# Kernel optimization log

Measured on AMD Instinct MI355X. Metric: run time of the kernel, lower is better.

Reference implementation:

```python
import jax, jax.numpy as jnp
import numpy as np

N_USERS = 200000
N_ITEMS = 50000
N_ENTITIES = 150000
N_RELATIONS = 32
N_EDGES = 2000000
N_INTER = 1000000
N_HOPS = 2
D = 64


def setup_inputs() -> dict:
    key = jax.random.key(0)
    ks = jax.random.split(key, 10)
    return {
        "user_emb": jax.random.normal(ks[0], (N_USERS, D), jnp.float32) * 0.1,
        "entity_emb": jax.random.normal(ks[1], (N_ENTITIES, D), jnp.float32) * 0.1,
        "weight": jax.random.normal(ks[2], (N_RELATIONS, D), jnp.float32) * 0.1,
        "g1_w": jax.random.normal(ks[3], (D, D), jnp.float32) * 0.1,
        "g2_w": jax.random.normal(ks[4], (D, D), jnp.float32) * 0.1,
        "edge_head": jax.random.randint(ks[5], (N_EDGES,), 0, N_ENTITIES),
        "edge_tail": jax.random.randint(ks[6], (N_EDGES,), 0, N_ENTITIES),
        "edge_type": jax.random.randint(ks[7], (N_EDGES,), 0, N_RELATIONS),
        "mat_row": jax.random.randint(ks[8], (N_INTER,), 0, N_USERS),
        "mat_col": jax.random.randint(ks[9], (N_INTER,), 0, N_ITEMS),
    }


def _scatter_mean(src, index, num_segments):
    s = jax.ops.segment_sum(src, index, num_segments=num_segments)
    cnt = jax.ops.segment_sum(jnp.ones((src.shape[0],), src.dtype), index,
                              num_segments=num_segments)
    return s / jnp.maximum(cnt, 1.0)[:, None]


def _l2norm(x, eps=1e-12):
    n = jnp.sqrt(jnp.sum(x * x, axis=-1, keepdims=True))
    return x / jnp.maximum(n, eps)


def reference(user_emb, entity_emb, weight, g1_w, g2_w,
              edge_head, edge_tail, edge_type, mat_row, mat_col):
    entity_res = entity_emb
    user_res = user_emb
    item_kg_res = jnp.zeros((N_ITEMS, D), entity_emb.dtype)
    item_int_res = jnp.zeros((N_ITEMS, D), entity_emb.dtype)

    for _ in range(N_HOPS):
        # KG aggregation: gather tail embs, modulate by relation emb, scatter-mean to head
        neigh = entity_emb[edge_tail] * weight[edge_type]            # [E, D]
        entity_agg = _scatter_mean(neigh, edge_head, N_ENTITIES)      # [n_ent, D]
        item_kg_agg = entity_agg[:N_ITEMS]
        att_kg_agg = entity_agg[N_ITEMS:]
        # interaction aggregation: mean of user embs per item
        item_int_agg = _scatter_mean(user_emb[mat_row], mat_col, N_ITEMS)
        # gated fusion (F.linear: x @ W.T)
        gi = jax.nn.sigmoid(item_kg_agg @ g1_w.T + item_int_agg @ g2_w.T)
        item_fusion = gi * item_kg_agg + (1.0 - gi) * item_int_agg
        # user_agg = sparse.mm(user_item, item_fusion) == segment-sum over rows
        user_agg = jax.ops.segment_sum(item_fusion[mat_col], mat_row,
                                       num_segments=N_USERS)
        entity_emb = _l2norm(jnp.concatenate([item_fusion, att_kg_agg], axis=0))
        user_emb = _l2norm(user_agg)
        item_kg_n = _l2norm(item_kg_agg)
        item_int_n = _l2norm(item_int_agg)
        entity_res = entity_res + entity_emb
        user_res = user_res + user_emb
        item_kg_res = item_kg_res + item_kg_n
        item_int_res = item_int_res + item_int_n

    return (entity_res, user_res, item_kg_res, item_int_res)
```

## Files before the change

### kernel.cpp

```cpp
#include <hip/hip_runtime.h>
#include <math.h>

#define N_USERS    200000
#define N_ITEMS    50000
#define N_ENTITIES 150000
#define N_EDGES    2000000
#define N_INTER    1000000
#define D          64

#define CHUNK      1250
#define THR_OWN    5
#define NBLK_E     120
#define NBLK_C     40
#define NBLK_R     160
#define NBLK_TOT   (NBLK_E + NBLK_C + NBLK_R)

#define RK     16384
#define NS     16
#define NR_E   10
#define NR_C   4
#define NR_R   13
#define NR_TOT (NR_E + NR_C + NR_R)
#define KTOT   (N_ENTITIES + N_ITEMS + N_USERS)

#define EB     2048
#define IB     1024

#define FT    64
#define FPAD  132
#define NTILE ((N_ITEMS + FT - 1) / FT)

__device__ __forceinline__ unsigned short f2bf(float f) {
    unsigned u = __float_as_uint(f);
    u += 0x7FFFu + ((u >> 16) & 1u);
    return (unsigned short)(u >> 16);
}
__device__ __forceinline__ ushort4 f2bf4(float4 f) {
    ushort4 o;
    o.x = f2bf(f.x); o.y = f2bf(f.y); o.z = f2bf(f.z); o.w = f2bf(f.w);
    return o;
}
__device__ __forceinline__ float4 bf2f4(ushort4 h) {
    float4 f;
    f.x = __uint_as_float(((unsigned)h.x) << 16);
    f.y = __uint_as_float(((unsigned)h.y) << 16);
    f.z = __uint_as_float(((unsigned)h.z) << 16);
    f.w = __uint_as_float(((unsigned)h.w) << 16);
    return f;
}

__device__ __forceinline__ float qsum16(float v) {
#pragma unroll
    for (int off = 1; off < 16; off <<= 1) v += __shfl_xor(v, off, 64);
    return v;
}

__global__ void cvt2_k(const float4* __restrict__ a, ushort4* __restrict__ ab, int na4,
                       const float4* __restrict__ b, ushort4* __restrict__ bb, int nb4) {
    int n = na4 + nb4;
    for (int i = blockIdx.x * blockDim.x + threadIdx.x; i < n;
         i += gridDim.x * blockDim.x) {
        if (i < na4) ab[i] = f2bf4(a[i]);
        else         bb[i - na4] = f2bf4(b[i - na4]);
    }
}

__global__ void pack_k(const int* __restrict__ tail, const int* __restrict__ type,
                       int* __restrict__ packed) {
    for (int i = blockIdx.x * blockDim.x + threadIdx.x; i < N_EDGES;
         i += gridDim.x * blockDim.x) {
        packed[i] = tail[i] | (type[i] << 18);
    }
}

__device__ __forceinline__ void range_geom(int r, const int*& src, int& n,
                                           int& base, int& cbase, int& rlen,
                                           const int* head, const int* mcol,
                                           const int* mrow) {
    if (r < NR_E) {
        src = head; n = N_EDGES; base = r * RK; cbase = 0;
        rlen = N_ENTITIES - base;
    } else if (r < NR_E + NR_C) {
        src = mcol; n = N_INTER; base = (r - NR_E) * RK;
        cbase = N_ENTITIES; rlen = N_ITEMS - base;
    } else {
        src = mrow; n = N_INTER; base = (r - NR_E - NR_C) * RK;
        cbase = N_ENTITIES + N_ITEMS; rlen = N_USERS - base;
    }
    if (rlen > RK) rlen = RK;
}

__global__ void hist_part_k(const int* __restrict__ head,
                            const int* __restrict__ mcol,
                            const int* __restrict__ mrow,
                            int* __restrict__ partial) {
    __shared__ int lh[RK];
    int r = blockIdx.x >> 4, s = blockIdx.x & (NS - 1);
    for (int d = threadIdx.x; d < RK; d += 256) lh[d] = 0;
    __syncthreads();
    const int* src; int n, base, cbase, rlen;
    range_geom(r, src, n, base, cbase, rlen, head, mcol, mrow);
    int chunk = n / NS;
    int lo = s * chunk, hi = lo + chunk;
    int i = lo + threadIdx.x;
    for (; i + 768 < hi; i += 1024) {
        unsigned d0 = (unsigned)(__builtin_nontemporal_load(&src[i])       - base);
        unsigned d1 = (unsigned)(__builtin_nontemporal_load(&src[i + 256]) - base);
        unsigned d2 = (unsigned)(__builtin_nontemporal_load(&src[i + 512]) - base);
        unsigned d3 = (unsigned)(__builtin_nontemporal_load(&src[i + 768]) - base);
        if (d0 < (unsigned)RK) atomicAdd(&lh[d0], 1);
        if (d1 < (unsigned)RK) atomicAdd(&lh[d1], 1);
        if (d2 < (unsigned)RK) atomicAdd(&lh[d2], 1);
        if (d3 < (unsigned)RK) atomicAdd(&lh[d3], 1);
    }
    for (; i < hi; i += 256) {
        unsigned d = (unsigned)(__builtin_nontemporal_load(&src[i]) - base);
        if (d < (unsigned)RK) atomicAdd(&lh[d], 1);
    }
    __syncthreads();
    int* dst = partial + (size_t)s * KTOT + cbase + base;
    for (int d = threadIdx.x; d < rlen; d += 256) dst[d] = lh[d];
}

__global__ void scanA_k(const int* __restrict__ partial,
                        int* __restrict__ blk_sums) {
    __shared__ int ss[256];
    int b = blockIdx.x, t = threadIdx.x;
    int base = b * CHUNK;
    int sum = 0;
    if (t < 250) {
        int g = base + t * THR_OWN;
#pragma unroll
        for (int s = 0; s < NS; ++s) {
            const int* p = partial + (size_t)s * KTOT + g;
#pragma unroll
            for (int j = 0; j < THR_OWN; ++j) sum += p[j];
        }
    }
    ss[t] = sum;
    __syncthreads();
    for (int off = 128; off > 0; off >>= 1) {
        if (t < off) ss[t] += ss[t + off];
        __syncthreads();
    }
    if (t == 0) blk_sums[b] = ss[0];
}

__global__ void scanB_k(int* __restrict__ blk_sums, int* __restrict__ blk_off,
                        int* __restrict__ e_starts, int* __restrict__ c_starts,
                        int* __restrict__ r_starts) {
    __shared__ int ss[512];
    int t = threadIdx.x;
    ss[t] = (t < NBLK_TOT) ? blk_sums[t] : 0;
    __syncthreads();
    for (int off = 1; off < 512; off <<= 1) {
        int v = (t >= off) ? ss[t - off] : 0;
        __syncthreads();
        ss[t] += v;
        __syncthreads();
    }
    if (t < NBLK_TOT) {
        int excl = (t == 0) ? 0 : ss[t - 1];
        int segstart_excl;
        if (t < NBLK_E) segstart_excl = 0;
        else if (t < NBLK_E + NBLK_C) segstart_excl = ss[NBLK_E - 1];
        else segstart_excl = ss[NBLK_E + NBLK_C - 1];
        blk_off[t] = excl - segstart_excl;
    }
    if (t == 0) {
        e_starts[N_ENTITIES] = N_EDGES;
        c_starts[N_ITEMS]    = N_INTER;
        r_starts[N_USERS]    = N_INTER;
    }
}

__global__ void scanC_k(const int* __restrict__ partial,
                        const int* __restrict__ blk_off,
                        int* __restrict__ e_starts, int* __restrict__ c_starts,
                        int* __restrict__ r_starts,
                        int* __restrict__ e_curs, int* __restrict__ c_curs,
                        int* __restrict__ r_curs) {
    __shared__ int ss[256];
    int b = blockIdx.x, t = threadIdx.x;
    int base = b * CHUNK;
    int tot[THR_OWN];
    int sum = 0;
    if (t < 250) {
        int g = base + t * THR_OWN;
#pragma unroll
        for (int j = 0; j < THR_OWN; ++j) tot[j] = 0;
#pragma unroll
        for (int s = 0; s < NS; ++s) {
            const int* p = partial + (size_t)s * KTOT + g;
#pragma unroll
            for (int j = 0; j < THR_OWN; ++j) tot[j] += p[j];
        }
#pragma unroll
        for (int j = 0; j < THR_OWN; ++j) sum += tot[j];
    }
    ss[t] = sum;
    __syncthreads();
    for (int off = 1; off < 256; off <<= 1) {
        int v = (t >= off) ? ss[t - off] : 0;
        __syncthreads();
        ss[t] += v;
        __syncthreads();
    }
    if (t < 250) {
        int run = blk_off[b] + ((t == 0) ? 0 : ss[t - 1]);
        int* sarr; int* carr; int ebase;
        if (b < NBLK_E)               { sarr = e_starts; carr = e_curs; ebase = base; }
        else if (b < NBLK_E + NBLK_C) { sarr = c_starts; carr = c_curs; ebase = base - NBLK_E * CHUNK; }
        else                          { sarr = r_starts; carr = r_curs; ebase = base - (NBLK_E + NBLK_C) * CHUNK; }
        int gl = ebase + t * THR_OWN;
#pragma unroll
        for (int j = 0; j < THR_OWN; ++j) {
            sarr[gl + j] = run;
            carr[gl + j] = run;
            run += tot[j];
        }
    }
}

__global__ void permute_e_k(const int* __restrict__ head,
                            const int* __restrict__ packed,
                            int* __restrict__ ec, int* __restrict__ e_sorted) {
    int xcd = blockIdx.x & 7;
    int slot = blockIdx.x >> 3;
    int nslot = gridDim.x >> 3;
    int lo = xcd * (N_ENTITIES / 8);
    int hi = lo + (N_ENTITIES / 8);
    for (int i = slot * blockDim.x + threadIdx.x; i < N_EDGES;
         i += nslot * blockDim.x) {
        int h = __builtin_nontemporal_load(&head[i]);
        if (h >= lo && h < hi) {
            int pos = atomicAdd(&ec[h], 1);
            e_sorted[pos] = __builtin_nontemporal_load(&packed[i]);
        }
    }
}

__global__ void permute_i_k(const int* __restrict__ mcol, const int* __restrict__ mrow,
                            int* __restrict__ cc, int* __restrict__ rc,
                            int* __restrict__ i_srow, int* __restrict__ i_scol) {
    int xcd = blockIdx.x & 7;
    int slot = blockIdx.x >> 3;
    int nslot = gridDim.x >> 3;
    int clo = xcd * (N_ITEMS / 8), chi = clo + (N_ITEMS / 8);
    int rlo = xcd * (N_USERS / 8), rhi = rlo + (N_USERS / 8);
    for (int i = slot * blockDim.x + threadIdx.x; i < N_INTER;
         i += nslot * blockDim.x) {
        int c = __builtin_nontemporal_load(&mcol[i]);
        int r = __builtin_nontemporal_load(&mrow[i]);
        if (c >= clo && c < chi) {
            int pos = atomicAdd(&cc[c], 1);
            i_srow[pos] = r;
        }
        if (r >= rlo && r < rhi) {
            int pos = atomicAdd(&rc[r], 1);
            i_scol[pos] = c;
        }
    }
}

__global__ void agg_all_k(const ushort4* __restrict__ ent_bf,
                          const float* __restrict__ ent0f,
                          const float* __restrict__ wrel,
                          const int* __restrict__ es,
                          const int* __restrict__ e_sorted,
                          float* __restrict__ agg,
                          ushort4* __restrict__ ent_cur_bf,
                          float* __restrict__ ent_res,
                          const ushort4* __restrict__ usr_bf,
                          const int* __restrict__ cs,
                          const int* __restrict__ i_srow,
                          float* __restrict__ iint,
                          int first) {
    int lane = threadIdx.x & 63;
    int q = lane >> 4, ql = lane & 15;
    int qb = lane & 48;
    if (blockIdx.x < EB) {
        __shared__ float4 wl4[32 * 16];
        for (int idx = threadIdx.x; idx < 512; idx += 256)
            wl4[idx] = ((const float4*)wrel)[idx];
        __syncthreads();
        int qid = (blockIdx.x * 4 + (threadIdx.x >> 6)) * 4 + q;
        int nq = EB * 16;
        for (int h = qid; h < N_ENTITIES; h += nq) {
            int beg = es[h], end = es[h + 1];
            float4 a0 = {0, 0, 0, 0}, a1 = {0, 0, 0, 0};
            for (int j0 = beg; j0 < end; j0 += 16) {
                int p = (j0 + ql < end) ? e_sorted[j0 + ql] : 0;
                int mm = end - j0; if (mm > 16) mm = 16;
                int k = 0;
                for (; k + 1 < mm; k += 2) {
                    int p0 = __shfl(p, qb | k, 64);
                    int p1 = __shfl(p, qb | (k + 1), 64);
                    float4 e0 = bf2f4(ent_bf[(size_t)(p0 & 0x3FFFF) * 16 + ql]);
                    float4 w0 = wl4[((p0 >> 18) << 4) + ql];
                    float4 e1 = bf2f4(ent_bf[(size_t)(p1 & 0x3FFFF) * 16 + ql]);
                    float4 w1 = wl4[((p1 >> 18) << 4) + ql];
                    a0.x = fmaf(e0.x, w0.x, a0.x); a0.y = fmaf(e0.y, w0.y, a0.y);
                    a0.z = fmaf(e0.z, w0.z, a0.z); a0.w = fmaf(e0.w, w0.w, a0.w);
                    a1.x = fmaf(e1.x, w1.x, a1.x); a1.y = fmaf(e1.y, w1.y, a1.y);
                    a1.z = fmaf(e1.z, w1.z, a1.z); a1.w = fmaf(e1.w, w1.w, a1.w);
                }
                if (k < mm) {
                    int p0 = __shfl(p, qb | k, 64);
                    float4 e0 = bf2f4(ent_bf[(size_t)(p0 & 0x3FFFF) * 16 + ql]);
                    float4 w0 = wl4[((p0 >> 18) << 4) + ql];
                    a0.x = fmaf(e0.x, w0.x, a0.x); a0.y = fmaf(e0.y, w0.y, a0.y);
                    a0.z = fmaf(e0.z, w0.z, a0.z); a0.w = fmaf(e0.w, w0.w, a0.w);
                }
            }
            float4 v; v.x = a0.x + a1.x; v.y = a0.y + a1.y;
            v.z = a0.z + a1.z; v.w = a0.w + a1.w;
            if (h < N_ITEMS) {
                int d = end - beg;
                float inv = 1.0f / (float)(d > 0 ? d : 1);
                float4 o; o.x = v.x * inv; o.y = v.y * inv;
                o.z = v.z * inv; o.w = v.w * inv;
                ((float4*)agg)[(size_t)h * 16 + ql] = o;
            } else {
                float s = qsum16(fmaf(v.x, v.x, fmaf(v.y, v.y, fmaf(v.z, v.z, v.w * v.w))));
                float inv = 1.0f / fmaxf(sqrtf(s), 1e-12f);
                float4 vn; vn.x = v.x * inv; vn.y = v.y * inv;
                vn.z = v.z * inv; vn.w = v.w * inv;
                size_t o4 = (size_t)h * 16 + ql;
                if (first) {
                    ent_cur_bf[o4] = f2bf4(vn);
                    float4 b = ((const float4*)ent0f)[o4];
                    b.x += vn.x; b.y += vn.y; b.z += vn.z; b.w += vn.w;
                    ((float4*)ent_res)[o4] = b;
                } else {
                    float4 r = ((float4*)ent_res)[o4];
                    r.x += vn.x; r.y += vn.y; r.z += vn.z; r.w += vn.w;
                    ((float4*)ent_res)[o4] = r;
                }
            }
        }
    } else {
        int qid = ((blockIdx.x - EB) * 4 + (threadIdx.x >> 6)) * 4 + q;
        int nq = IB * 16;
        for (int c = qid; c < N_ITEMS; c += nq) {
            int beg = cs[c], end = cs[c + 1];
            float4 a0 = {0, 0, 0, 0}, a1 = {0, 0, 0, 0};
            for (int j0 = beg; j0 < end; j0 += 16) {
                int p = (j0 + ql < end) ? i_srow[j0 + ql] : 0;
                int mm = end - j0; if (mm > 16) mm = 16;
                int k = 0;
                for (; k + 1 < mm; k += 2) {
                    int p0 = __shfl(p, qb | k, 64);
                    int p1 = __shfl(p, qb | (k + 1), 64);
                    float4 u0 = bf2f4(usr_bf[(size_t)p0 * 16 + ql]);
                    float4 u1 = bf2f4(usr_bf[(size_t)p1 * 16 + ql]);
                    a0.x += u0.x; a0.y += u0.y; a0.z += u0.z; a0.w += u0.w;
                    a1.x += u1.x; a1.y += u1.y; a1.z += u1.z; a1.w += u1.w;
                }
                if (k < mm) {
                    int p0 = __shfl(p, qb | k, 64);
                    float4 u0 = bf2f4(usr_bf[(size_t)p0 * 16 + ql]);
                    a0.x += u0.x; a0.y += u0.y; a0.z += u0.z; a0.w += u0.w;
                }
            }
            float4 v; v.x = a0.x + a1.x; v.y = a0.y + a1.y;
            v.z = a0.z + a1.z; v.w = a0.w + a1.w;
            int d = end - beg;
            float inv = 1.0f / (float)(d > 0 ? d : 1);
            float4 o; o.x = v.x * inv; o.y = v.y * inv;
            o.z = v.z * inv; o.w = v.w * inv;
            ((float4*)iint)[(size_t)c * 16 + ql] = o;
        }
    }
}

__global__ void fuse_k(const float* __restrict__ agg,
                       const float* __restrict__ iint,
                       const float* __restrict__ g1,
                       const float* __restrict__ g2,
                       const float* __restrict__ ent0,
                       unsigned short* __restrict__ ifus_bf,
                       unsigned short* __restrict__ ent_cur_bf,
                       float* __restrict__ ent_res,
                       float* __restrict__ kg_res,
                       float* __restrict__ int_res,
                       int first) {
    __shared__ float A[FT * FPAD];
    __shared__ float B[64 * FPAD];
    int t = threadIdx.x;
    int ibase = blockIdx.x * FT;

    {
        const float4* g14 = (const float4*)g1;
        const float4* g24 = (const float4*)g2;
        const float4* a4 = (const float4*)(agg + (size_t)ibase * D);
        const float4* i4 = (const float4*)(iint + (size_t)ibase * D);
        for (int idx = t; idx < 1024; idx += 256) {
            int r = idx >> 4, kq = idx & 15;
            ((float4*)&B[r * FPAD])[kq]      = g14[idx];
            ((float4*)&B[r * FPAD + 64])[kq] = g24[idx];
            ((float4*)&A[r * FPAD])[kq]      = a4[idx];
            ((float4*)&A[r * FPAD + 64])[kq] = i4[idx];
        }
    }
    __syncthreads();

    int ti = t >> 4, tj = t & 15;

    float y[4][4] = {};
    for (int k = 0; k < 128; k += 4) {
        float4 av[4], bv[4];
#pragma unroll
        for (int a = 0; a < 4; ++a) av[a] = *(const float4*)&A[(ti + 16 * a) * FPAD + k];
#pragma unroll
        for (int b = 0; b < 4; ++b) bv[b] = *(const float4*)&B[(tj + 16 * b) * FPAD + k];
#pragma unroll
        for (int a = 0; a < 4; ++a)
#pragma unroll
            for (int b = 0; b < 4; ++b) {
                y[a][b] = fmaf(av[a].x, bv[b].x, y[a][b]);
                y[a][b] = fmaf(av[a].y, bv[b].y, y[a][b]);
                y[a][b] = fmaf(av[a].z, bv[b].z, y[a][b]);
                y[a][b] = fmaf(av[a].w, bv[b].w, y[a][b]);
            }
    }

    float fus[4][4], kg[4][4], ii[4][4];
    float sf[4], sk[4], si[4];
#pragma unroll
    for (int a = 0; a < 4; ++a) { sf[a] = 0.f; sk[a] = 0.f; si[a] = 0.f; }
#pragma unroll
    for (int a = 0; a < 4; ++a) {
        int i = ti + 16 * a;
#pragma unroll
        for (int b = 0; b < 4; ++b) {
            int j = tj + 16 * b;
            float K = A[i * FPAD + j];
            float I = A[i * FPAD + 64 + j];
            float gi = 1.0f / (1.0f + __expf(-y[a][b]));
            float f = gi * K + (1.0f - gi) * I;
            fus[a][b] = f; kg[a][b] = K; ii[a][b] = I;
            sf[a] = fmaf(f, f, sf[a]);
            sk[a] = fmaf(K, K, sk[a]);
            si[a] = fmaf(I, I, si[a]);
        }
    }
#pragma unroll
    for (int off = 1; off < 16; off <<= 1) {
#pragma unroll
        for (int a = 0; a < 4; ++a) {
            sf[a] += __shfl_xor(sf[a], off, 64);
            sk[a] += __shfl_xor(sk[a], off, 64);
            si[a] += __shfl_xor(si[a], off, 64);
        }
    }

#pragma unroll
    for (int a = 0; a < 4; ++a) {
        int i = ibase + ti + 16 * a;
        if (i < N_ITEMS) {
            float nf = 1.0f / fmaxf(sqrtf(sf[a]), 1e-12f);
            float nk = 1.0f / fmaxf(sqrtf(sk[a]), 1e-12f);
            float ni = 1.0f / fmaxf(sqrtf(si[a]), 1e-12f);
#pragma unroll
            for (int b = 0; b < 4; ++b) {
                size_t o = (size_t)i * D + tj + 16 * b;
                float f = fus[a][b];
                ifus_bf[o] = f2bf(f);
                float fn = f * nf;
                ent_cur_bf[o] = f2bf(fn);
                if (first) {
                    ent_res[o] = ent0[o] + fn;
                    kg_res[o]  = kg[a][b] * nk;
                    int_res[o] = ii[a][b] * ni;
                } else {
                    ent_res[o] += fn;
                    kg_res[o]  += kg[a][b] * nk;
                    int_res[o] += ii[a][b] * ni;
                }
            }
        }
    }
}

__global__ void user_agg_k(const ushort4* __restrict__ ifus_bf,
                           const int* __restrict__ rs,
                           const int* __restrict__ i_scol,
                           const float* __restrict__ usr0,
                           ushort4* __restrict__ usr_cur_bf,
                           float* __restrict__ usr_res,
                           int first) {
    const float4* u04 = (const float4*)usr0;
    int lane = threadIdx.x & 63;
    int q = lane >> 4, ql = lane & 15;
    int qb = lane & 48;
    int qid = (blockIdx.x * (blockDim.x >> 6) + (threadIdx.x >> 6)) * 4 + q;
    int nq = gridDim.x * (blockDim.x >> 6) * 4;
    for (int u = qid; u < N_USERS; u += nq) {
        int beg = rs[u], end = rs[u + 1];
        float4 a0 = {0, 0, 0, 0}, a1 = {0, 0, 0, 0};
        for (int j0 = beg; j0 < end; j0 += 16) {
            int p = (j0 + ql < end) ? i_scol[j0 + ql] : 0;
            int mm = end - j0; if (mm > 16) mm = 16;
            int k = 0;
            for (; k + 1 < mm; k += 2) {
                int p0 = __shfl(p, qb | k, 64);
                int p1 = __shfl(p, qb | (k + 1), 64);
                float4 u0 = bf2f4(ifus_bf[(size_t)p0 * 16 + ql]);
                float4 u1 = bf2f4(ifus_bf[(size_t)p1 * 16 + ql]);
                a0.x += u0.x; a0.y += u0.y; a0.z += u0.z; a0.w += u0.w;
                a1.x += u1.x; a1.y += u1.y; a1.z += u1.z; a1.w += u1.w;
            }
            if (k < mm) {
                int p0 = __shfl(p, qb | k, 64);
                float4 u0 = bf2f4(ifus_bf[(size_t)p0 * 16 + ql]);
                a0.x += u0.x; a0.y += u0.y; a0.z += u0.z; a0.w += u0.w;
            }
        }
        float4 v; v.x = a0.x + a1.x; v.y = a0.y + a1.y;
        v.z = a0.z + a1.z; v.w = a0.w + a1.w;
        float s = qsum16(fmaf(v.x, v.x, fmaf(v.y, v.y, fmaf(v.z, v.z, v.w * v.w))));
        float inv = 1.0f / fmaxf(sqrtf(s), 1e-12f);
        float4 vn; vn.x = v.x * inv; vn.y = v.y * inv;
        vn.z = v.z * inv; vn.w = v.w * inv;
        size_t o4 = (size_t)u * 16 + ql;
        usr_cur_bf[o4] = f2bf4(vn);
        if (first) {
            float4 b = u04[o4];
            b.x += vn.x; b.y += vn.y; b.z += vn.z; b.w += vn.w;
            ((float4*)usr_res)[o4] = b;
        } else {
            float4 r = ((float4*)usr_res)[o4];
            r.x += vn.x; r.y += vn.y; r.z += vn.z; r.w += vn.w;
            ((float4*)usr_res)[o4] = r;
        }
    }
}

extern "C" void kernel_launch(void* const* d_in, const int* in_sizes, int n_in,
                              void* d_out, int out_size, void* d_ws, size_t ws_size,
                              hipStream_t stream) {
    const float* user_emb   = (const float*)d_in[0];
    const float* entity_emb = (const float*)d_in[1];
    const float* wrel       = (const float*)d_in[2];
    const float* g1         = (const float*)d_in[3];
    const float* g2         = (const float*)d_in[4];
    const int*   edge_head  = (const int*)d_in[5];
    const int*   edge_tail  = (const int*)d_in[6];
    const int*   edge_type  = (const int*)d_in[7];
    const int*   mat_row    = (const int*)d_in[8];
    const int*   mat_col    = (const int*)d_in[9];

    const size_t ENT_SZ = (size_t)N_ENTITIES * D;
    const size_t USR_SZ = (size_t)N_USERS * D;
    const size_t ITM_SZ = (size_t)N_ITEMS * D;

    float* out     = (float*)d_out;
    float* ent_res = out;
    float* usr_res = out + ENT_SZ;
    float* kg_res  = out + ENT_SZ + USR_SZ;
    float* int_res = out + ENT_SZ + USR_SZ + ITM_SZ;

    char* p = (char*)d_ws;
    unsigned short* ent_cur_bf = (unsigned short*)p; p += ENT_SZ * 2;
    unsigned short* usr_cur_bf = (unsigned short*)p; p += USR_SZ * 2;
    unsigned short* ent0_bf    = (unsigned short*)p; p += ENT_SZ * 2;
    unsigned short* usr0_bf    = (unsigned short*)p; p += USR_SZ * 2;
    float* agg  = (float*)p; p += ITM_SZ * 4;
    float* iint = (float*)p; p += ITM_SZ * 4;
    unsigned short* ifus_bf = (unsigned short*)p; p += ITM_SZ * 2;
    int* e_starts = (int*)p; p += (N_ENTITIES + 1) * 4;
    int* c_starts = (int*)p; p += (N_ITEMS + 1) * 4;
    int* r_starts = (int*)p; p += (N_USERS + 1) * 4;
    int* e_curs   = (int*)p; p += N_ENTITIES * 4;
    int* c_curs   = (int*)p; p += N_ITEMS * 4;
    int* r_curs   = (int*)p; p += N_USERS * 4;
    p = (char*)(((size_t)p + 15) & ~(size_t)15);
    int* e_sorted = (int*)p; p += (size_t)N_EDGES * 4;
    int* i_srow   = (int*)p; p += (size_t)N_INTER * 4;
    int* i_scol   = (int*)p; p += (size_t)N_INTER * 4;
    int* packed   = (int*)p; p += (size_t)N_EDGES * 4;
    int* blk_sums = (int*)p; p += NBLK_TOT * 4;
    int* blk_off  = (int*)p; p += NBLK_TOT * 4;
    int* partial = (int*)agg;

    cvt2_k<<<2048, 256, 0, stream>>>((const float4*)entity_emb, (ushort4*)ent0_bf,
                                     (int)(ENT_SZ / 4),
                                     (const float4*)user_emb, (ushort4*)usr0_bf,
                                     (int)(USR_SZ / 4));
    pack_k<<<1024, 256, 0, stream>>>(edge_tail, edge_type, packed);

    hist_part_k<<<NR_TOT * NS, 256, 0, stream>>>(edge_head, mat_col, mat_row, partial);
    scanA_k<<<NBLK_TOT, 256, 0, stream>>>(partial, blk_sums);
    scanB_k<<<1, 512, 0, stream>>>(blk_sums, blk_off, e_starts, c_starts, r_starts);
    scanC_k<<<NBLK_TOT, 256, 0, stream>>>(partial, blk_off,
                                          e_starts, c_starts, r_starts,
                                          e_curs, c_curs, r_curs);
    permute_e_k<<<4096, 256, 0, stream>>>(edge_head, packed, e_curs, e_sorted);
    permute_i_k<<<4096, 256, 0, stream>>>(mat_col, mat_row,
                                          c_curs, r_curs, i_srow, i_scol);

    for (int hop = 0; hop < 2; ++hop) {
        const unsigned short* ent_src = (hop == 0) ? ent0_bf : ent_cur_bf;
        const unsigned short* usr_src = (hop == 0) ? usr0_bf : usr_cur_bf;
        int first = (hop == 0);
        agg_all_k<<<EB + IB, 256, 0, stream>>>((const ushort4*)ent_src, entity_emb,
                                               wrel, e_starts, e_sorted,
                                               agg, (ushort4*)ent_cur_bf, ent_res,
                                               (const ushort4*)usr_src, c_starts,
                                               i_srow, iint, first);
        fuse_k<<<NTILE, 256, 0, stream>>>(agg, iint, g1, g2, entity_emb,
                                          ifus_bf, ent_cur_bf,
                                          ent_res, kg_res, int_res, first);
        user_agg_k<<<2048, 256, 0, stream>>>((const ushort4*)ifus_bf, r_starts,
                                             i_scol, user_emb,
                                             (ushort4*)usr_cur_bf, usr_res, first);
    }
}
```

Measured before the change: 612.8 us.

## Replace global-atomic permutation with per-slice LDS cursor counting-sort scatter

The scan kernel now turns the per-slice histogram partials into exclusive per-slice offsets written back in place. A single fused permute kernel then loads each (range, slice) cursor block into LDS and scatters edges and interactions using shared-memory atomics. This replaces the two global-atomic permute kernels and their cursor arrays, cutting global atomic traffic and one launch. The trade-off is extra read/write passes over the partials in the scan and a 64KB LDS footprint per block, which limits occupancy.

```diff
diff --git a/kernel.cpp b/kernel.cpp
--- a/kernel.cpp
+++ b/kernel.cpp
@@ -22,6 +22,7 @@
 #define NR_R   13
 #define NR_TOT (NR_E + NR_C + NR_R)
 #define KTOT   (N_ENTITIES + N_ITEMS + N_USERS)
+#define PERM_GRID (8 * NS * 4)
 
 #define EB     2048
 #define IB     1024
@@ -76,15 +77,15 @@
 __device__ __forceinline__ void range_geom(int r, const int*& src, int& n,
                                            int& base, int& cbase, int& rlen,
                                            const int* head, const int* mcol,
-                                           const int* mrow) {
+                                           const int* mrow, int& which) {
     if (r < NR_E) {
-        src = head; n = N_EDGES; base = r * RK; cbase = 0;
+        which = 0; src = head; n = N_EDGES; base = r * RK; cbase = 0;
         rlen = N_ENTITIES - base;
     } else if (r < NR_E + NR_C) {
-        src = mcol; n = N_INTER; base = (r - NR_E) * RK;
+        which = 1; src = mcol; n = N_INTER; base = (r - NR_E) * RK;
         cbase = N_ENTITIES; rlen = N_ITEMS - base;
     } else {
-        src = mrow; n = N_INTER; base = (r - NR_E - NR_C) * RK;
+        which = 2; src = mrow; n = N_INTER; base = (r - NR_E - NR_C) * RK;
         cbase = N_ENTITIES + N_ITEMS; rlen = N_USERS - base;
     }
     if (rlen > RK) rlen = RK;
@@ -98,8 +99,8 @@
     int r = blockIdx.x >> 4, s = blockIdx.x & (NS - 1);
     for (int d = threadIdx.x; d < RK; d += 256) lh[d] = 0;
     __syncthreads();
-    const int* src; int n, base, cbase, rlen;
-    range_geom(r, src, n, base, cbase, rlen, head, mcol, mrow);
+    const int* src; int n, base, cbase, rlen, which;
+    range_geom(r, src, n, base, cbase, rlen, head, mcol, mrow, which);
     int chunk = n / NS;
     int lo = s * chunk, hi = lo + chunk;
     int i = lo + threadIdx.x;
@@ -174,12 +175,10 @@
     }
 }
 
-__global__ void scanC_k(const int* __restrict__ partial,
+__global__ void scanC_k(int* __restrict__ partial,
                         const int* __restrict__ blk_off,
                         int* __restrict__ e_starts, int* __restrict__ c_starts,
-                        int* __restrict__ r_starts,
-                        int* __restrict__ e_curs, int* __restrict__ c_curs,
-                        int* __restrict__ r_curs) {
+                        int* __restrict__ r_starts) {
     __shared__ int ss[256];
     int b = blockIdx.x, t = threadIdx.x;
     int base = b * CHUNK;
@@ -208,57 +207,94 @@
     }
     if (t < 250) {
         int run = blk_off[b] + ((t == 0) ? 0 : ss[t - 1]);
-        int* sarr; int* carr; int ebase;
-        if (b < NBLK_E)               { sarr = e_starts; carr = e_curs; ebase = base; }
-        else if (b < NBLK_E + NBLK_C) { sarr = c_starts; carr = c_curs; ebase = base - NBLK_E * CHUNK; }
-        else                          { sarr = r_starts; carr = r_curs; ebase = base - (NBLK_E + NBLK_C) * CHUNK; }
+        int* sarr; int ebase;
+        if (b < NBLK_E)               { sarr = e_starts; ebase = base; }
+        else if (b < NBLK_E + NBLK_C) { sarr = c_starts; ebase = base - NBLK_E * CHUNK; }
+        else                          { sarr = r_starts; ebase = base - (NBLK_E + NBLK_C) * CHUNK; }
         int gl = ebase + t * THR_OWN;
-#pragma unroll
+        int gg = base + t * THR_OWN;
         for (int j = 0; j < THR_OWN; ++j) {
             sarr[gl + j] = run;
-            carr[gl + j] = run;
-            run += tot[j];
-        }
-    }
-}
-
-__global__ void permute_e_k(const int* __restrict__ head,
-                            const int* __restrict__ packed,
-                            int* __restrict__ ec, int* __restrict__ e_sorted) {
-    int xcd = blockIdx.x & 7;
-    int slot = blockIdx.x >> 3;
-    int nslot = gridDim.x >> 3;
-    int lo = xcd * (N_ENTITIES / 8);
-    int hi = lo + (N_ENTITIES / 8);
-    for (int i = slot * blockDim.x + threadIdx.x; i < N_EDGES;
-         i += nslot * blockDim.x) {
-        int h = __builtin_nontemporal_load(&head[i]);
-        if (h >= lo && h < hi) {
-            int pos = atomicAdd(&ec[h], 1);
-            e_sorted[pos] = __builtin_nontemporal_load(&packed[i]);
-        }
-    }
-}
-
-__global__ void permute_i_k(const int* __restrict__ mcol, const int* __restrict__ mrow,
-                            int* __restrict__ cc, int* __restrict__ rc,
-                            int* __restrict__ i_srow, int* __restrict__ i_scol) {
-    int xcd = blockIdx.x & 7;
-    int slot = blockIdx.x >> 3;
-    int nslot = gridDim.x >> 3;
-    int clo = xcd * (N_ITEMS / 8), chi = clo + (N_ITEMS / 8);
-    int rlo = xcd * (N_USERS / 8), rhi = rlo + (N_USERS / 8);
-    for (int i = slot * blockDim.x + threadIdx.x; i < N_INTER;
-         i += nslot * blockDim.x) {
-        int c = __builtin_nontemporal_load(&mcol[i]);
-        int r = __builtin_nontemporal_load(&mrow[i]);
-        if (c >= clo && c < chi) {
-            int pos = atomicAdd(&cc[c], 1);
-            i_srow[pos] = r;
-        }
-        if (r >= rlo && r < rhi) {
-            int pos = atomicAdd(&rc[r], 1);
-            i_scol[pos] = c;
+            int cur = run;
+#pragma unroll
+            for (int s = 0; s < NS; ++s) {
+                int idx = s * KTOT + gg + j;
+                int v = partial[idx];
+                partial[idx] = cur;
+                cur += v;
+            }
+            run = cur;
+        }
+    }
+}
+
+__global__ void perm2_k(const int* __restrict__ head,
+                        const int* __restrict__ packed,
+                        const int* __restrict__ mcol, const int* __restrict__ mrow,
+                        const int* __restrict__ partial,
+                        int* __restrict__ e_sorted, int* __restrict__ i_srow,
+                        int* __restrict__ i_scol) {
+    __shared__ int lc[RK];
+    int xs = blockIdx.x & 7;
+    int rest = blockIdx.x >> 3;
+    int s = rest & (NS - 1);
+    int rgrp = rest >> 4;
+    int r = rgrp * 8 + xs;
+    if (r >= NR_TOT) return;
+    const int* src; int n, base, cbase, rlen, which;
+    range_geom(r, src, n, base, cbase, rlen, head, mcol, mrow, which);
+    const int* csrc = partial + (size_t)s * KTOT + cbase + base;
+    for (int d = threadIdx.x; d < rlen; d += 256) lc[d] = csrc[d];
+    __syncthreads();
+    int chunk = n / NS;
+    int lo = s * chunk, hi = lo + chunk;
+    if (which == 0) {
+        int i = lo + threadIdx.x;
+        for (; i + 768 < hi; i += 1024) {
+            unsigned d0 = (unsigned)(__builtin_nontemporal_load(&head[i])       - base);
+            unsigned d1 = (unsigned)(__builtin_nontemporal_load(&head[i + 256]) - base);
+            unsigned d2 = (unsigned)(__builtin_nontemporal_load(&head[i + 512]) - base);
+            unsigned d3 = (unsigned)(__builtin_nontemporal_load(&head[i + 768]) - base);
+            if (d0 < (unsigned)RK) e_sorted[atomicAdd(&lc[d0], 1)] = __builtin_nontemporal_load(&packed[i]);
+            if (d1 < (unsigned)RK) e_sorted[atomicAdd(&lc[d1], 1)] = __builtin_nontemporal_load(&packed[i + 256]);
+            if (d2 < (unsigned)RK) e_sorted[atomicAdd(&lc[d2], 1)] = __builtin_nontemporal_load(&packed[i + 512]);
+            if (d3 < (unsigned)RK) e_sorted[atomicAdd(&lc[d3], 1)] = __builtin_nontemporal_load(&packed[i + 768]);
+        }
+        for (; i < hi; i += 256) {
+            unsigned d = (unsigned)(__builtin_nontemporal_load(&head[i]) - base);
+            if (d < (unsigned)RK) e_sorted[atomicAdd(&lc[d], 1)] = __builtin_nontemporal_load(&packed[i]);
+        }
+    } else if (which == 1) {
+        int i = lo + threadIdx.x;
+        for (; i + 768 < hi; i += 1024) {
+            unsigned d0 = (unsigned)(__builtin_nontemporal_load(&mcol[i])       - base);
+            unsigned d1 = (unsigned)(__builtin_nontemporal_load(&mcol[i + 256]) - base);
+            unsigned d2 = (unsigned)(__builtin_nontemporal_load(&mcol[i + 512]) - base);
+            unsigned d3 = (unsigned)(__builtin_nontemporal_load(&mcol[i + 768]) - base);
+            if (d0 < (unsigned)RK) i_srow[atomicAdd(&lc[d0], 1)] = __builtin_nontemporal_load(&mrow[i]);
+            if (d1 < (unsigned)RK) i_srow[atomicAdd(&lc[d1], 1)] = __builtin_nontemporal_load(&mrow[i + 256]);
+            if (d2 < (unsigned)RK) i_srow[atomicAdd(&lc[d2], 1)] = __builtin_nontemporal_load(&mrow[i + 512]);
+            if (d3 < (unsigned)RK) i_srow[atomicAdd(&lc[d3], 1)] = __builtin_nontemporal_load(&mrow[i + 768]);
+        }
+        for (; i < hi; i += 256) {
+            unsigned d = (unsigned)(__builtin_nontemporal_load(&mcol[i]) - base);
+            if (d < (unsigned)RK) i_srow[atomicAdd(&lc[d], 1)] = __builtin_nontemporal_load(&mrow[i]);
+        }
+    } else {
+        int i = lo + threadIdx.x;
+        for (; i + 768 < hi; i += 1024) {
+            unsigned d0 = (unsigned)(__builtin_nontemporal_load(&mrow[i])       - base);
+            unsigned d1 = (unsigned)(__builtin_nontemporal_load(&mrow[i + 256]) - base);
+            unsigned d2 = (unsigned)(__builtin_nontemporal_load(&mrow[i + 512]) - base);
+            unsigned d3 = (unsigned)(__builtin_nontemporal_load(&mrow[i + 768]) - base);
+            if (d0 < (unsigned)RK) i_scol[atomicAdd(&lc[d0], 1)] = __builtin_nontemporal_load(&mcol[i]);
+            if (d1 < (unsigned)RK) i_scol[atomicAdd(&lc[d1], 1)] = __builtin_nontemporal_load(&mcol[i + 256]);
+            if (d2 < (unsigned)RK) i_scol[atomicAdd(&lc[d2], 1)] = __builtin_nontemporal_load(&mcol[i + 512]);
+            if (d3 < (unsigned)RK) i_scol[atomicAdd(&lc[d3], 1)] = __builtin_nontemporal_load(&mcol[i + 768]);
+        }
+        for (; i < hi; i += 256) {
+            unsigned d = (unsigned)(__builtin_nontemporal_load(&mrow[i]) - base);
+            if (d < (unsigned)RK) i_scol[atomicAdd(&lc[d], 1)] = __builtin_nontemporal_load(&mcol[i]);
         }
     }
 }
@@ -572,9 +608,6 @@
     int* e_starts = (int*)p; p += (N_ENTITIES + 1) * 4;
     int* c_starts = (int*)p; p += (N_ITEMS + 1) * 4;
     int* r_starts = (int*)p; p += (N_USERS + 1) * 4;
-    int* e_curs   = (int*)p; p += N_ENTITIES * 4;
-    int* c_curs   = (int*)p; p += N_ITEMS * 4;
-    int* r_curs   = (int*)p; p += N_USERS * 4;
     p = (char*)(((size_t)p + 15) & ~(size_t)15);
     int* e_sorted = (int*)p; p += (size_t)N_EDGES * 4;
     int* i_srow   = (int*)p; p += (size_t)N_INTER * 4;
@@ -594,11 +627,9 @@
     scanA_k<<<NBLK_TOT, 256, 0, stream>>>(partial, blk_sums);
     scanB_k<<<1, 512, 0, stream>>>(blk_sums, blk_off, e_starts, c_starts, r_starts);
     scanC_k<<<NBLK_TOT, 256, 0, stream>>>(partial, blk_off,
-                                          e_starts, c_starts, r_starts,
-                                          e_curs, c_curs, r_curs);
-    permute_e_k<<<4096, 256, 0, stream>>>(edge_head, packed, e_curs, e_sorted);
-    permute_i_k<<<4096, 256, 0, stream>>>(mat_col, mat_row,
-                                          c_curs, r_curs, i_srow, i_scol);
+                                          e_starts, c_starts, r_starts);
+    perm2_k<<<PERM_GRID, 256, 0, stream>>>(edge_head, packed, mat_col, mat_row,
+                                           partial, e_sorted, i_srow, i_scol);
 
     for (int hop = 0; hop < 2; ++hop) {
         const unsigned short* ent_src = (hop == 0) ? ent0_bf : ent_cur_bf;
```

Result: slower. 762.4 us (+24.4%).
